# Kernel optimization log

Hardware: AMD Instinct MI355X
Metric: run time of the kernel (lower is better)

The kernel has to match this reference:

```python
import jax, jax.numpy as jnp
import numpy as np

V, E, H = 512, 128, 256
B, S, T = 2048, 32, 48


def setup_inputs() -> dict:
    key = jax.random.key(0)
    ks = jax.random.split(key, 13)
    def p(i, shape):
        return jax.random.normal(ks[i], shape, dtype=jnp.float32) * 0.05
    return {
        "source": jax.random.randint(ks[0], (B, S), 0, V),
        "target_len": T,
        "enc_emb": p(1, (V, E)),
        "enc_Wih": p(2, (4 * H, E)),
        "enc_Whh": p(3, (4 * H, H)),
        "enc_bih": p(4, (4 * H,)),
        "enc_bhh": p(5, (4 * H,)),
        "dec_emb": p(6, (V, E)),
        "dec_Wih": p(7, (4 * H, E)),
        "dec_Whh": p(8, (4 * H, H)),
        "dec_bih": p(9, (4 * H,)),
        "dec_bhh": p(10, (4 * H,)),
        "fc_W": p(11, (V, H)),
        "fc_b": p(12, (V,)),
    }


def lstm_cell(x, h, c, Wih, Whh, bih, bhh):
    # torch gate order: i, f, g, o
    z = x @ Wih.T + h @ Whh.T + (bih + bhh)
    i, f, g, o = jnp.split(z, 4, axis=-1)
    c = jax.nn.sigmoid(f) * c + jax.nn.sigmoid(i) * jnp.tanh(g)
    h = jax.nn.sigmoid(o) * jnp.tanh(c)
    return h, c


def reference(source, target_len, enc_emb, enc_Wih, enc_Whh, enc_bih, enc_bhh,
              dec_emb, dec_Wih, dec_Whh, dec_bih, dec_bhh, fc_W, fc_b):
    Bsz = source.shape[0]
    Hd = enc_Whh.shape[1]
    h0 = jnp.zeros((Bsz, Hd), dtype=enc_emb.dtype)
    c0 = jnp.zeros((Bsz, Hd), dtype=enc_emb.dtype)

    # ---- encoder: embed whole source, scan single-layer LSTM over time ----
    emb_seq = jnp.swapaxes(enc_emb[source], 0, 1)  # [S, B, E]

    def enc_step(carry, x_t):
        h, c = carry
        h, c = lstm_cell(x_t, h, c, enc_Wih, enc_Whh, enc_bih, enc_bhh)
        return (h, c), None

    (h, c), _ = jax.lax.scan(enc_step, (h0, c0), emb_seq)

    sos = jnp.zeros((Bsz,), dtype=jnp.int32)  # char2idx.get('<SOS>', 0) == 0

    def dec_step(carry, _):
        tok, h, c = carry
        x = dec_emb[tok]                         # [B, E]
        h, c = lstm_cell(x, h, c, dec_Wih, dec_Whh, dec_bih, dec_bhh)
        logits = h @ fc_W.T + fc_b               # [B, V]
        nxt = jnp.argmax(logits, axis=-1).astype(jnp.int32)
        return (nxt, h, c), logits

    _, logits = jax.lax.scan(dec_step, (sos, h, c), None, length=target_len)
    return jnp.swapaxes(logits, 0, 1)            # [B, target_len, V]
```

## Files before the change

### kernel.cpp

```cpp
#include <hip/hip_runtime.h>
#include <cmath>

#define S_LEN 32
#define E_DIM 128
#define H_DIM 256
#define V_DIM 512
#define NTILE 18
#define W_TILES 12
#define TILE_SHORTS 8192
#define A_SHORTS 12288
#define ZPITCH 132

typedef _Float16 f16x8v __attribute__((ext_vector_type(8)));
typedef __attribute__((ext_vector_type(4))) float f32x4v;

#define SCALE_S 4096.0f
#define INV_S   2.44140625e-4f

__device__ __forceinline__ float sigf(float x) { return 1.0f / (1.0f + expf(-x)); }

template<int L>
__device__ __forceinline__ unsigned short lvl_f16(float x) {
  _Float16 h1 = (_Float16)x;
  if (L == 1) return __builtin_bit_cast(unsigned short, h1);
  _Float16 h2 = (_Float16)((x - (float)h1) * SCALE_S);
  return __builtin_bit_cast(unsigned short, h2);
}

__global__ void prep_weights(const float* __restrict__ eWih, const float* __restrict__ eWhh,
                             const float* __restrict__ dWih, const float* __restrict__ dWhh,
                             unsigned short* __restrict__ We, unsigned short* __restrict__ Wd,
                             float* __restrict__ h0, float* __restrict__ c,
                             int* __restrict__ tok)
{
  const int b = blockIdx.x;
  if (b >= 192) {
    const int pb = b - 192;
    const int gt = pb * 256 + threadIdx.x;
    float4 z = make_float4(0.f, 0.f, 0.f, 0.f);
    float4* p0 = (float4*)h0;
    float4* pc = (float4*)c;
    for (int i = gt; i < 131072; i += 16384) { p0[i] = z; pc[i] = z; }
    if (gt < 2048) tok[gt] = 0;
    return;
  }
  const int j    = b % W_TILES;
  const int rest = b / W_TILES;
  const int nb   = rest & 7;
  const int set  = rest >> 3;
  const float* Wih = set ? dWih : eWih;
  const float* Whh = set ? dWhh : eWhh;
  unsigned short* dst = (set ? Wd : We) + ((size_t)nb * W_TILES + j) * TILE_SHORTS;
  const int lvl = (j < 6) ? 1 : 2;
  const int jj  = (j < 6) ? j : j - 6;

  for (int cpos = threadIdx.x; cpos < 1024; cpos += 256) {
    int fi = cpos >> 6, l = cpos & 63;
    int kh = fi >> 3, wc = (fi >> 2) & 1, g = fi & 3;
    int n  = g * H_DIM + nb * 32 + wc * 16 + (l & 15);
    int kk = jj * 64 + kh * 32 + (l >> 4) * 8;
    unsigned short o8[8];
    #pragma unroll
    for (int e = 0; e < 8; ++e) {
      int k = kk + e;
      float v = (k < E_DIM) ? Wih[(size_t)n * E_DIM + k]
                            : Whh[(size_t)n * H_DIM + (k - E_DIM)];
      o8[e] = (lvl == 1) ? lvl_f16<1>(v) : lvl_f16<2>(v);
    }
    uint4 pk;
    pk.x = (unsigned)o8[0] | ((unsigned)o8[1] << 16);
    pk.y = (unsigned)o8[2] | ((unsigned)o8[3] << 16);
    pk.z = (unsigned)o8[4] | ((unsigned)o8[5] << 16);
    pk.w = (unsigned)o8[6] | ((unsigned)o8[7] << 16);
    *(uint4*)&dst[(size_t)cpos * 8] = pk;
  }
}

__device__ __forceinline__ void stage_A12(unsigned short* Ax1, unsigned short* Ax2,
                                          const float* __restrict__ esrc,
                                          const float* __restrict__ hsrc,
                                          int arow, int q8) {
  const int rowblk = arow >> 4;
  const int rlo    = arow & 15;
  #pragma unroll
  for (int j = 0; j < 12; ++j) {
    int k0, kA;
    const float* src;
    if (j < 4) { kA = q8 * 4 + 32 * j;            src = esrc + kA; }
    else       { k0 = q8 * 4 + 32 * (j - 4); kA = E_DIM + k0; src = hsrc + k0; }
    float4 v = *(const float4*)src;
    _Float16 a1x = (_Float16)v.x, a1y = (_Float16)v.y,
             a1z = (_Float16)v.z, a1w = (_Float16)v.w;
    _Float16 a2x = (_Float16)((v.x - (float)a1x) * SCALE_S);
    _Float16 a2y = (_Float16)((v.y - (float)a1y) * SCALE_S);
    _Float16 a2z = (_Float16)((v.z - (float)a1z) * SCALE_S);
    _Float16 a2w = (_Float16)((v.w - (float)a1w) * SCALE_S);
    int lane_w = rlo + ((kA & 31) >> 3) * 16;
    int idx = (((kA >> 5) * 2 + rowblk) * 64 + lane_w) * 8 + (kA & 7);
    uint2 p1, p2;
    p1.x = (unsigned)__builtin_bit_cast(unsigned short, a1x)
         | ((unsigned)__builtin_bit_cast(unsigned short, a1y) << 16);
    p1.y = (unsigned)__builtin_bit_cast(unsigned short, a1z)
         | ((unsigned)__builtin_bit_cast(unsigned short, a1w) << 16);
    p2.x = (unsigned)__builtin_bit_cast(unsigned short, a2x)
         | ((unsigned)__builtin_bit_cast(unsigned short, a2y) << 16);
    p2.y = (unsigned)__builtin_bit_cast(unsigned short, a2z)
         | ((unsigned)__builtin_bit_cast(unsigned short, a2w) << 16);
    *(uint2*)&Ax1[idx] = p1;
    *(uint2*)&Ax2[idx] = p2;
  }
}

__launch_bounds__(256, 2)
__global__ void lstm_mfma_kernel(const float* __restrict__ emb,
                                 const int* __restrict__ idx_src, int idx_stride, int idx_off,
                                 const unsigned short* __restrict__ Wf,
                                 const float* __restrict__ bih, const float* __restrict__ bhh,
                                 const float* __restrict__ h_in,
                                 float* __restrict__ h_out, float* __restrict__ c)
{
  __shared__ __align__(16) unsigned short Ax1[A_SHORTS];
  __shared__ __align__(16) unsigned short Ax2[A_SHORTS];

  const int tid  = threadIdx.x;
  const int lane = tid & 63;
  const int m0 = blockIdx.x * 32;
  const int nb = blockIdx.y;
  const int nc0 = nb * 32;

  const int arow = tid >> 3;
  const int q8   = tid & 7;
  const int token = idx_src[(size_t)(m0 + arow) * idx_stride + idx_off];
  const float* esrc = emb + (size_t)token * E_DIM;
  const float* hsrc = h_in + (size_t)(m0 + arow) * H_DIM;

  const int wm = (tid >> 6) & 1;
  const int wc = tid >> 7;
  const int lr = tid & 15;
  const int l4 = lane >> 4;

  const unsigned short* wbase = Wf + (size_t)nb * (W_TILES * TILE_SHORTS)
                                   + (size_t)(wc * 4) * 512 + (size_t)lane * 8;

  f32x4v accA[4], accB[4];
  #pragma unroll
  for (int g = 0; g < 4; ++g) {
    accA[g] = (f32x4v){0.f, 0.f, 0.f, 0.f};
    accB[g] = (f32x4v){0.f, 0.f, 0.f, 0.f};
  }

  uint4 pA[8], pB[8], pC[8], pD[8];

#define LOADT(J, P)                                                            \
  {                                                                            \
    const unsigned short* bsrc =                                               \
        wbase + (size_t)(((J) < W_TILES) ? (J) : (J) - W_TILES) * TILE_SHORTS; \
    _Pragma("unroll")                                                          \
    for (int f = 0; f < 4; ++f) {                                              \
      P[f]     = *(const uint4*)(bsrc + (size_t)f * 512);                      \
      P[4 + f] = *(const uint4*)(bsrc + (size_t)(8 + f) * 512);                \
    }                                                                          \
  }

#define MFMAT(J, P, ACC, AXB)                                                  \
  {                                                                            \
    const int ks0 = ((J) % 6) * 2;                                             \
    _Pragma("unroll")                                                          \
    for (int kh = 0; kh < 2; ++kh) {                                           \
      f16x8v af = *(const f16x8v*)&AXB[((ks0 + kh) * 2 + wm) * 512 + lane * 8]; \
      _Pragma("unroll")                                                        \
      for (int g = 0; g < 4; ++g) {                                            \
        f16x8v bfr = __builtin_bit_cast(f16x8v, P[kh * 4 + g]);                \
        ACC[g] = __builtin_amdgcn_mfma_f32_16x16x32_f16(af, bfr, ACC[g], 0, 0, 0); \
      }                                                                        \
    }                                                                          \
  }

  LOADT(0, pA); LOADT(1, pB); LOADT(2, pC);

  stage_A12(Ax1, Ax2, esrc, hsrc, arow, q8);
  asm volatile("s_waitcnt lgkmcnt(0)" ::: "memory");
  __builtin_amdgcn_s_barrier();

  LOADT(3, pD);  MFMAT(0, pA, accA, Ax1);
  LOADT(4, pA);  MFMAT(1, pB, accA, Ax1);
  LOADT(5, pB);  MFMAT(2, pC, accA, Ax1);
  LOADT(6, pC);  MFMAT(3, pD, accA, Ax1);
  LOADT(7, pD);  MFMAT(4, pA, accA, Ax1);
  LOADT(8, pA);  MFMAT(5, pB, accA, Ax1);
  LOADT(9, pB);  MFMAT(6, pC, accB, Ax1);
  LOADT(10, pC); MFMAT(7, pD, accB, Ax1);
  LOADT(11, pD); MFMAT(8, pA, accB, Ax1);
  LOADT(12, pA); MFMAT(9, pB, accB, Ax1);
  LOADT(13, pB); MFMAT(10, pC, accB, Ax1);
  LOADT(14, pC); MFMAT(11, pD, accB, Ax1);
  LOADT(15, pD); MFMAT(12, pA, accB, Ax2);
  LOADT(16, pA); MFMAT(13, pB, accB, Ax2);
  LOADT(17, pB); MFMAT(14, pC, accB, Ax2);

  const int er = tid >> 3;
  const int ec = tid & 7;
  const float* cp0 = c + (size_t)(m0 + er) * H_DIM + nc0 + ec * 4;
  float4 cold = *(const float4*)(cp0);

  MFMAT(15, pD, accB, Ax2);
  MFMAT(16, pA, accB, Ax2);
  MFMAT(17, pB, accB, Ax2);

#undef LOADT
#undef MFMAT

  float bs[4];
  #pragma unroll
  for (int g = 0; g < 4; ++g)
    bs[g] = bih[g * H_DIM + nc0 + wc * 16 + lr] + bhh[g * H_DIM + nc0 + wc * 16 + lr];

  float* zb = (float*)Ax1;
  asm volatile("s_waitcnt lgkmcnt(0)" ::: "memory");
  __builtin_amdgcn_s_barrier();

  #pragma unroll
  for (int r = 0; r < 4; ++r) {
    int row_l = wm * 16 + l4 * 4 + r;
    int base = row_l * ZPITCH + (wc * 16 + lr) * 4;
    #pragma unroll
    for (int g = 0; g < 4; ++g)
      zb[base + g] = fmaf(accB[g][r], INV_S, accA[g][r]) + bs[g];
  }

  asm volatile("s_waitcnt lgkmcnt(0)" ::: "memory");
  __builtin_amdgcn_s_barrier();

  {
    float* hp  = h_out + (size_t)(m0 + er) * H_DIM + nc0 + ec * 4;
    float* cpw = (float*)cp0;
    float cov[4] = {cold.x, cold.y, cold.z, cold.w};
    float cnv[4], hnv[4];
    #pragma unroll
    for (int cc = 0; cc < 4; ++cc) {
      float4 zq = *(const float4*)&zb[er * ZPITCH + (ec * 4 + cc) * 4];
      float zi = zq.x, zf = zq.y, zg = zq.z, zo = zq.w;
      float cn = sigf(zf) * cov[cc] + sigf(zi) * tanhf(zg);
      cnv[cc] = cn;
      hnv[cc] = sigf(zo) * tanhf(cn);
    }
    *(float4*)cpw = make_float4(cnv[0], cnv[1], cnv[2], cnv[3]);
    *(float4*)hp  = make_float4(hnv[0], hnv[1], hnv[2], hnv[3]);
  }
}

__launch_bounds__(256)
__global__ void declog_kernel(const float* __restrict__ h,
                              const float* __restrict__ fcW,
                              const float* __restrict__ fcb,
                              float* __restrict__ out,
                              int* __restrict__ tok,
                              int t, int T)
{
  __shared__ float bv[8][256];
  __shared__ int   bi[8][256];

  const int tid  = threadIdx.x;
  const int lane = tid & 63;
  const int wv   = tid >> 6;
  const int r0   = blockIdx.x * 8;
  const int c0   = tid * 2;

  const float* hb  = h + (size_t)r0 * H_DIM;
  const float* w0p = fcW + (size_t)c0 * H_DIM;
  const float* w1p = w0p + H_DIM;

  float acc[8][2] = {};

  #pragma unroll 1
  for (int k0 = 0; k0 < H_DIM; k0 += 16) {
    float4 b0[4], b1[4];
    #pragma unroll
    for (int q = 0; q < 4; ++q) {
      b0[q] = *(const float4*)(w0p + k0 + q * 4);
      b1[q] = *(const float4*)(w1p + k0 + q * 4);
    }
    #pragma unroll
    for (int q = 0; q < 4; ++q) {
      #pragma unroll
      for (int r = 0; r < 8; ++r) {
        float4 a = *(const float4*)(hb + (size_t)r * H_DIM + k0 + q * 4);
        acc[r][0] = fmaf(a.x, b0[q].x, acc[r][0]);
        acc[r][0] = fmaf(a.y, b0[q].y, acc[r][0]);
        acc[r][0] = fmaf(a.z, b0[q].z, acc[r][0]);
        acc[r][0] = fmaf(a.w, b0[q].w, acc[r][0]);
        acc[r][1] = fmaf(a.x, b1[q].x, acc[r][1]);
        acc[r][1] = fmaf(a.y, b1[q].y, acc[r][1]);
        acc[r][1] = fmaf(a.z, b1[q].z, acc[r][1]);
        acc[r][1] = fmaf(a.w, b1[q].w, acc[r][1]);
      }
    }
  }

  const float fb0 = fcb[c0];
  const float fb1 = fcb[c0 + 1];
  #pragma unroll
  for (int r = 0; r < 8; ++r) {
    float z0 = acc[r][0] + fb0;
    float z1 = acc[r][1] + fb1;
    *(float2*)(out + (size_t)(r0 + r) * T * V_DIM + (size_t)t * V_DIM + c0)
        = make_float2(z0, z1);
    float v = z0; int ix = c0;
    if (z1 > v) { v = z1; ix = c0 + 1; }
    bv[r][tid] = v;
    bi[r][tid] = ix;
  }
  __syncthreads();

  #pragma unroll
  for (int rr = 0; rr < 2; ++rr) {
    int r = wv * 2 + rr;
    float best = bv[r][lane];
    int   bidx = bi[r][lane];
    #pragma unroll
    for (int s = 1; s < 4; ++s) {
      float ov = bv[r][lane + 64 * s];
      int   oi = bi[r][lane + 64 * s];
      if (ov > best || (ov == best && oi < bidx)) { best = ov; bidx = oi; }
    }
    #pragma unroll
    for (int off = 32; off; off >>= 1) {
      float ov = __shfl_xor(best, off);
      int   oi = __shfl_xor(bidx, off);
      if (ov > best || (ov == best && oi < bidx)) { best = ov; bidx = oi; }
    }
    if (lane == 0) tok[r0 + r] = bidx;
  }
}

extern "C" void kernel_launch(void* const* d_in, const int* in_sizes, int n_in,
                              void* d_out, int out_size, void* d_ws, size_t ws_size,
                              hipStream_t stream) {
  const int*   source  = (const int*)d_in[0];
  const float* enc_emb = (const float*)d_in[2];
  const float* enc_Wih = (const float*)d_in[3];
  const float* enc_Whh = (const float*)d_in[4];
  const float* enc_bih = (const float*)d_in[5];
  const float* enc_bhh = (const float*)d_in[6];
  const float* dec_emb = (const float*)d_in[7];
  const float* dec_Wih = (const float*)d_in[8];
  const float* dec_Whh = (const float*)d_in[9];
  const float* dec_bih = (const float*)d_in[10];
  const float* dec_bhh = (const float*)d_in[11];
  const float* fc_W    = (const float*)d_in[12];
  const float* fc_b    = (const float*)d_in[13];
  float* out = (float*)d_out;

  const int B = in_sizes[0] / S_LEN;
  const int T = out_size / (B * V_DIM);

  const size_t BH = (size_t)B * H_DIM;
  const size_t WFSZ = (size_t)8 * W_TILES * TILE_SHORTS;
  float* h0  = (float*)d_ws;
  float* h1  = h0 + BH;
  float* c   = h1 + BH;
  int*   tok = (int*)(c + BH);
  unsigned short* We = (unsigned short*)(tok + B);
  unsigned short* Wd = We + WFSZ;

  prep_weights<<<dim3(192 + 64), dim3(256), 0, stream>>>(
      enc_Wih, enc_Whh, dec_Wih, dec_Whh, We, Wd, h0, c, tok);

  dim3 blk(256);
  dim3 g_lstm(B / 32, H_DIM / 32);
  dim3 g_declog(B / 8);

  const float* hin = h0;
  float* hout = h1;

  for (int s = 0; s < S_LEN; ++s) {
    lstm_mfma_kernel<<<g_lstm, blk, 0, stream>>>(
        enc_emb, source, S_LEN, s, We, enc_bih, enc_bhh, hin, hout, c);
    const float* tmp = hout; hout = (float*)hin; hin = tmp;
  }

  for (int t = 0; t < T; ++t) {
    lstm_mfma_kernel<<<g_lstm, blk, 0, stream>>>(
        dec_emb, tok, 1, 0, Wd, dec_bih, dec_bhh, hin, hout, c);
    const float* tmp = hout; hout = (float*)hin; hin = tmp;
    declog_kernel<<<g_declog, blk, 0, stream>>>(hin, fc_W, fc_b, out, tok, t, T);
  }
}
```

Measured before the change: 1.980 ms.

## Switch LSTM gate GEMM from 16x16x32 to 32x32x16 MFMA tiles

Reworks the per-step LSTM gate matmul so each wave computes one gate's 32x32 output tile with the 32x32x16 f16 MFMA instead of four 16x16x32 MFMAs across gates. The weight pre-pack and the shared-memory A layout are reordered to match the new operand fragment layout, and the per-wave weight prefetch shrinks from 8 to 4 vectors per tile. This cuts the MFMA instruction count and the register pressure from prefetch buffers. In exchange, the LDS gate scatter becomes scalar stores with a different bank pattern.

```diff
diff --git a/kernel.cpp b/kernel.cpp
--- a/kernel.cpp
+++ b/kernel.cpp
@@ -12,7 +12,7 @@
 #define ZPITCH 132
 
 typedef _Float16 f16x8v __attribute__((ext_vector_type(8)));
-typedef __attribute__((ext_vector_type(4))) float f32x4v;
+typedef float f32x16 __attribute__((ext_vector_type(16)));
 
 #define SCALE_S 4096.0f
 #define INV_S   2.44140625e-4f
@@ -56,9 +56,9 @@
 
   for (int cpos = threadIdx.x; cpos < 1024; cpos += 256) {
     int fi = cpos >> 6, l = cpos & 63;
-    int kh = fi >> 3, wc = (fi >> 2) & 1, g = fi & 3;
-    int n  = g * H_DIM + nb * 32 + wc * 16 + (l & 15);
-    int kk = jj * 64 + kh * 32 + (l >> 4) * 8;
+    int g = fi >> 2, kc = fi & 3;
+    int n  = g * H_DIM + nb * 32 + (l & 31);
+    int kk = jj * 64 + kc * 16 + (l >> 5) * 8;
     unsigned short o8[8];
     #pragma unroll
     for (int e = 0; e < 8; ++e) {
@@ -80,8 +80,6 @@
                                           const float* __restrict__ esrc,
                                           const float* __restrict__ hsrc,
                                           int arow, int q8) {
-  const int rowblk = arow >> 4;
-  const int rlo    = arow & 15;
   #pragma unroll
   for (int j = 0; j < 12; ++j) {
     int k0, kA;
@@ -95,8 +93,8 @@
     _Float16 a2y = (_Float16)((v.y - (float)a1y) * SCALE_S);
     _Float16 a2z = (_Float16)((v.z - (float)a1z) * SCALE_S);
     _Float16 a2w = (_Float16)((v.w - (float)a1w) * SCALE_S);
-    int lane_w = rlo + ((kA & 31) >> 3) * 16;
-    int idx = (((kA >> 5) * 2 + rowblk) * 64 + lane_w) * 8 + (kA & 7);
+    int lane_w = arow + ((kA >> 3) & 1) * 32;
+    int idx = (((kA >> 4)) * 64 + lane_w) * 8 + (kA & 7);
     uint2 p1, p2;
     p1.x = (unsigned)__builtin_bit_cast(unsigned short, a1x)
          | ((unsigned)__builtin_bit_cast(unsigned short, a1y) << 16);
@@ -119,11 +117,13 @@
                                  const float* __restrict__ h_in,
                                  float* __restrict__ h_out, float* __restrict__ c)
 {
-  __shared__ __align__(16) unsigned short Ax1[A_SHORTS];
-  __shared__ __align__(16) unsigned short Ax2[A_SHORTS];
+  __shared__ __align__(16) unsigned short smem[2 * A_SHORTS];
+  unsigned short* Ax1 = smem;
+  unsigned short* Ax2 = smem + A_SHORTS;
 
   const int tid  = threadIdx.x;
   const int lane = tid & 63;
+  const int w    = tid >> 6;
   const int m0 = blockIdx.x * 32;
   const int nb = blockIdx.y;
   const int nc0 = nb * 32;
@@ -134,45 +134,34 @@
   const float* esrc = emb + (size_t)token * E_DIM;
   const float* hsrc = h_in + (size_t)(m0 + arow) * H_DIM;
 
-  const int wm = (tid >> 6) & 1;
-  const int wc = tid >> 7;
-  const int lr = tid & 15;
-  const int l4 = lane >> 4;
+  const int col32 = lane & 31;
+  const int lhi   = lane >> 5;
 
   const unsigned short* wbase = Wf + (size_t)nb * (W_TILES * TILE_SHORTS)
-                                   + (size_t)(wc * 4) * 512 + (size_t)lane * 8;
-
-  f32x4v accA[4], accB[4];
-  #pragma unroll
-  for (int g = 0; g < 4; ++g) {
-    accA[g] = (f32x4v){0.f, 0.f, 0.f, 0.f};
-    accB[g] = (f32x4v){0.f, 0.f, 0.f, 0.f};
-  }
-
-  uint4 pA[8], pB[8], pC[8], pD[8];
+                                   + (size_t)(w * 4) * 512 + (size_t)lane * 8;
+
+  f32x16 accA, accB;
+  #pragma unroll
+  for (int r = 0; r < 16; ++r) { accA[r] = 0.f; accB[r] = 0.f; }
+
+  uint4 pA[4], pB[4], pC[4], pD[4];
 
 #define LOADT(J, P)                                                            \
   {                                                                            \
     const unsigned short* bsrc =                                               \
         wbase + (size_t)(((J) < W_TILES) ? (J) : (J) - W_TILES) * TILE_SHORTS; \
     _Pragma("unroll")                                                          \
-    for (int f = 0; f < 4; ++f) {                                              \
-      P[f]     = *(const uint4*)(bsrc + (size_t)f * 512);                      \
-      P[4 + f] = *(const uint4*)(bsrc + (size_t)(8 + f) * 512);                \
-    }                                                                          \
-  }
-
-#define MFMAT(J, P, ACC, AXB)                                                  \
+    for (int kc = 0; kc < 4; ++kc) P[kc] = *(const uint4*)(bsrc + (size_t)kc * 512); \
+  }
+
+#define MFMAT(J, P, ACCX, AXB)                                                 \
   {                                                                            \
-    const int ks0 = ((J) % 6) * 2;                                             \
+    const int jj = ((J) < 6) ? (J) : (((J) < 12) ? (J) - 6 : (J) - 12);        \
     _Pragma("unroll")                                                          \
-    for (int kh = 0; kh < 2; ++kh) {                                           \
-      f16x8v af = *(const f16x8v*)&AXB[((ks0 + kh) * 2 + wm) * 512 + lane * 8]; \
-      _Pragma("unroll")                                                        \
-      for (int g = 0; g < 4; ++g) {                                            \
-        f16x8v bfr = __builtin_bit_cast(f16x8v, P[kh * 4 + g]);                \
-        ACC[g] = __builtin_amdgcn_mfma_f32_16x16x32_f16(af, bfr, ACC[g], 0, 0, 0); \
-      }                                                                        \
+    for (int kc = 0; kc < 4; ++kc) {                                           \
+      f16x8v af = *(const f16x8v*)&AXB[(jj * 4 + kc) * 512 + lane * 8];        \
+      f16x8v bfr = __builtin_bit_cast(f16x8v, P[kc]);                          \
+      ACCX = __builtin_amdgcn_mfma_f32_32x32x16_f16(af, bfr, ACCX, 0, 0, 0);   \
     }                                                                          \
   }
 
@@ -210,22 +199,16 @@
 #undef LOADT
 #undef MFMAT
 
-  float bs[4];
-  #pragma unroll
-  for (int g = 0; g < 4; ++g)
-    bs[g] = bih[g * H_DIM + nc0 + wc * 16 + lr] + bhh[g * H_DIM + nc0 + wc * 16 + lr];
-
-  float* zb = (float*)Ax1;
+  const float bsv = bih[w * H_DIM + nc0 + col32] + bhh[w * H_DIM + nc0 + col32];
+
+  float* zb = (float*)smem;
   asm volatile("s_waitcnt lgkmcnt(0)" ::: "memory");
   __builtin_amdgcn_s_barrier();
 
   #pragma unroll
-  for (int r = 0; r < 4; ++r) {
-    int row_l = wm * 16 + l4 * 4 + r;
-    int base = row_l * ZPITCH + (wc * 16 + lr) * 4;
-    #pragma unroll
-    for (int g = 0; g < 4; ++g)
-      zb[base + g] = fmaf(accB[g][r], INV_S, accA[g][r]) + bs[g];
+  for (int r = 0; r < 16; ++r) {
+    int row_l = (r & 3) + 8 * (r >> 2) + 4 * lhi;
+    zb[row_l * ZPITCH + col32 * 4 + w] = fmaf(accB[r], INV_S, accA[r]) + bsv;
   }
 
   asm volatile("s_waitcnt lgkmcnt(0)" ::: "memory");
```

Result: faster. 1.777 ms (-10.2%).
